# Kernel tuning notes

Hardware: AMD Instinct MI355X
Metric: run time of the kernel (lower is better)

The kernel has to match this reference:

```python
import jax, jax.numpy as jnp
import numpy as np

B, CIN, H, W = 4, 64, 128, 128
COUT, KH, KW = 64, 3, 3
STRIDE, PAD, DIL = 1, 1, 1
GROUPS, DG = 1, 1


def setup_inputs() -> dict:
    key = jax.random.key(0)
    k1, k2, k3, k4 = jax.random.split(key, 4)
    K = KH * KW
    x = jax.random.normal(k1, (B, CIN, H, W), jnp.float32)
    offset = jax.random.normal(k2, (B, 2 * DG * K, H, W), jnp.float32)
    mask = jax.random.uniform(k3, (B, DG * K, H, W), jnp.float32)
    stdv = 1.0 / np.sqrt(CIN * KH * KW)
    weight = jax.random.uniform(k4, (COUT, CIN // GROUPS, KH, KW), jnp.float32, -stdv, stdv)
    bias = jnp.zeros((COUT,), jnp.float32)
    return {"x": x, "offset": offset, "mask": mask, "weight": weight, "bias": bias}


def _deform_conv2d(x, offset, mask, weight, bias):
    Bn, C, Hi, Wi = x.shape
    Co, Cg_in, kh, kw = weight.shape
    K = kh * kw
    Ho = (Hi + 2 * PAD - DIL * (kh - 1) - 1) // STRIDE + 1
    Wo = (Wi + 2 * PAD - DIL * (kw - 1) - 1) // STRIDE + 1
    Cg = C // DG  # channels per deform group

    # offset channel layout: (deform_group, tap, {dy, dx})
    off = offset.reshape(Bn, DG, K, 2, Ho, Wo)
    dy, dx = off[:, :, :, 0], off[:, :, :, 1]          # [B, DG, K, Ho, Wo]
    m = mask.reshape(Bn, DG, K, Ho, Wo)

    ky = (jnp.arange(K) // kw) * DIL                    # tap row offsets
    kx = (jnp.arange(K) % kw) * DIL                     # tap col offsets
    oy = jnp.arange(Ho) * STRIDE - PAD
    ox = jnp.arange(Wo) * STRIDE - PAD
    py = dy + ky[None, None, :, None, None] + oy[None, None, None, :, None]
    px = dx + kx[None, None, :, None, None] + ox[None, None, None, None, :]

    y0f = jnp.floor(py)
    x0f = jnp.floor(px)
    wy = py - y0f
    wx = px - x0f
    y0 = y0f.astype(jnp.int32)
    x0 = x0f.astype(jnp.int32)

    xf = x.reshape(Bn, DG, Cg, Hi * Wi)

    def gather(yi, xi):
        # bilinear corner gather with zero padding outside the image
        valid = ((yi >= 0) & (yi < Hi) & (xi >= 0) & (xi < Wi)).astype(x.dtype)
        idx = jnp.clip(yi, 0, Hi - 1) * Wi + jnp.clip(xi, 0, Wi - 1)
        idx = jnp.broadcast_to(idx.reshape(Bn, DG, 1, -1), (Bn, DG, Cg, K * Ho * Wo))
        g = jnp.take_along_axis(xf, idx, axis=-1)
        return g.reshape(Bn, DG, Cg, K, Ho, Wo) * valid[:, :, None]

    v = (gather(y0, x0) * ((1 - wy) * (1 - wx))[:, :, None]
         + gather(y0, x0 + 1) * ((1 - wy) * wx)[:, :, None]
         + gather(y0 + 1, x0) * (wy * (1 - wx))[:, :, None]
         + gather(y0 + 1, x0 + 1) * (wy * wx)[:, :, None])
    v = v * m[:, :, None]                               # modulation, [B, DG, Cg, K, Ho, Wo]

    v = v.reshape(Bn, GROUPS, C // GROUPS, K, Ho, Wo)
    wflat = weight.reshape(GROUPS, Co // GROUPS, Cg_in, K)
    out = jnp.einsum('bgckhw,gock->bgohw', v, wflat).reshape(Bn, Co, Ho, Wo)
    return out + bias[None, :, None, None]


def reference(x, offset, mask, weight, bias):
    return _deform_conv2d(x, offset, mask, weight, bias)
```

## Files before the change

### kernel.cpp

```cpp
#include <hip/hip_runtime.h>

#define B_    4
#define CIN_  64
#define H_    128
#define W_    128
#define COUT_ 64
#define HW    (H_*W_)
#define KPOS  576

typedef __attribute__((ext_vector_type(8))) short    bf16x8;
typedef __attribute__((ext_vector_type(4))) short    bf16x4;
typedef __attribute__((ext_vector_type(4))) float    f32x4;
typedef __attribute__((ext_vector_type(4))) _Float16 f16x4;
typedef __attribute__((ext_vector_type(8))) _Float16 f16x8;

static __device__ __forceinline__ unsigned short f2bf(float f) {
    union { float f; unsigned u; } a; a.f = f;
    unsigned r = a.u + 0x7fffu + ((a.u >> 16) & 1u);
    return (unsigned short)(r >> 16);
}
static __device__ __forceinline__ float bfl(unsigned u) {
    union { unsigned x; float f; } a; a.x = u << 16; return a.f;
}

#define XT_HALFS   4194304
#define WP_HALFS   36864
#define META_CNT   (B_*9*HW)
#define OFFS_BYTE  ((XT_HALFS + WP_HALFS) * 2)
#define WTS_BYTE   (OFFS_BYTE + META_CNT * 4)
#define WS_NEED3   ((size_t)(WTS_BYTE + META_CNT * 8))

__global__ __launch_bounds__(256)
void prep_all(const float* __restrict__ x,
              const float* __restrict__ offset,
              const float* __restrict__ mask,
              const float* __restrict__ w,
              _Float16* __restrict__ xT,
              _Float16* __restrict__ wt,
              unsigned* __restrict__ mOffs,
              f16x4* __restrict__ mWts)
{
    const int bid = blockIdx.x;
    const int t   = threadIdx.x;

    if (bid < 512) {
        __shared__ _Float16 ld[64 * 132];
        const int b = bid >> 7;
        const int y = bid & 127;
        const float* src = x + (size_t)b * 64 * HW + y * W_;
        #pragma unroll
        for (int i = 0; i < 8; ++i) {
            const int e4 = (t + i * 256) * 4;
            const int c  = e4 >> 7;
            const int x0 = e4 & 127;
            const float4 v = *(const float4*)(src + (size_t)c * HW + x0);
            _Float16* d = &ld[c * 132 + x0];
            d[0] = (_Float16)v.x; d[1] = (_Float16)v.y;
            d[2] = (_Float16)v.z; d[3] = (_Float16)v.w;
        }
        __syncthreads();
        _Float16* dst = xT + ((size_t)b * HW + (size_t)y * W_) * 64;
        #pragma unroll
        for (int i = 0; i < 4; ++i) {
            const int o    = (t + i * 256) * 8;
            const int xcol = o >> 6;
            const int c0   = o & 63;
            union { f16x8 v; _Float16 u[8]; } pk;
            #pragma unroll
            for (int j = 0; j < 8; ++j) pk.u[j] = ld[(c0 + j) * 132 + xcol];
            *(f16x8*)(dst + o) = pk.v;
        }
    } else if (bid < 2816) {
        const int i  = (bid - 512) * 256 + t;
        const int gp = i & (HW - 1);
        const int bk = i >> 14;
        const int b  = bk / 9;
        const int k  = bk - b * 9;
        const int ho = gp >> 7, wo = gp & 127;
        const float dy = offset[(size_t)(b * 18 + 2 * k) * HW + gp];
        const float dx = offset[(size_t)(b * 18 + 2 * k + 1) * HW + gp];
        const float mm = mask[(size_t)bk * HW + gp];
        const float py  = dy + (float)(k / 3) + (float)(ho - 1);
        const float pxx = dx + (float)(k % 3) + (float)(wo - 1);
        const float y0f = floorf(py), x0f = floorf(pxx);
        const float wy = py - y0f, wx = pxx - x0f;
        const int y0 = (int)y0f, x0 = (int)x0f;
        const int y1 = y0 + 1,  x1 = x0 + 1;
        const bool vy0 = (y0 >= 0) & (y0 < H_), vy1 = (y1 >= 0) & (y1 < H_);
        const bool vx0 = (x0 >= 0) & (x0 < W_), vx1 = (x1 >= 0) & (x1 < W_);
        const int cy0 = min(max(y0, 0), H_-1), cy1 = min(max(y1, 0), H_-1);
        const int cx0 = min(max(x0, 0), W_-1), cx1 = min(max(x1, 0), W_-1);
        mOffs[i] = (unsigned)cy0 | ((unsigned)cy1 << 8)
                 | ((unsigned)cx0 << 16) | ((unsigned)cx1 << 24);
        f16x4 wv;
        wv[0] = (_Float16)((vy0 && vx0) ? (1.f - wy) * (1.f - wx) * mm : 0.f);
        wv[1] = (_Float16)((vy0 && vx1) ? (1.f - wy) * wx * mm         : 0.f);
        wv[2] = (_Float16)((vy1 && vx0) ? wy * (1.f - wx) * mm         : 0.f);
        wv[3] = (_Float16)((vy1 && vx1) ? wy * wx * mm                 : 0.f);
        mWts[i] = wv;
    } else {
        const int i = (bid - 2816) * 256 + t;
        if (i < 9 * 64 * 64) {
            const int k  = i >> 12;
            const int r  = i & 4095;
            const int co = r >> 6;
            const int c  = r & 63;
            wt[i] = (_Float16)w[co * KPOS + c * 9 + k];
        }
    }
}

__global__ __launch_bounds__(256, 4)
void dcn_f16(const _Float16* __restrict__ xT,
             const unsigned* __restrict__ mOffs,
             const f16x4* __restrict__ mWts,
             const float* __restrict__ bias,
             const _Float16* __restrict__ wprep,
             float* __restrict__ out)
{
    __shared__ _Float16 vP[2][64][72];
    __shared__ _Float16 Wk[2][64][72];

    const int t   = threadIdx.x;
    const int bid = blockIdx.x;
    const int wk  = ((bid & 7) << 7) | (bid >> 3);
    const int xh  = wk & 1;
    const int ho  = (wk >> 1) & 127;
    const int b   = wk >> 8;
    const int cq  = t >> 6;
    const int lane = t & 63;
    const int pxl  = lane >> 2;
    const int coct = lane & 3;

    f32x4 acc[4];
    #pragma unroll
    for (int i = 0; i < 4; ++i) acc[i] = (f32x4){0.f, 0.f, 0.f, 0.f};

    const _Float16* xTb = xT + (size_t)b * HW * 64;
    const int gp    = ho * W_ + xh * 64 + cq * 16 + pxl;
    const int mbase = (b * 9) << 14;

    unsigned pk9[9]; f16x4 wh9[9];
    #pragma unroll
    for (int k = 0; k < 9; ++k) {
        const int mi = mbase + (k << 14) + gp;
        pk9[k] = mOffs[mi];
        wh9[k] = mWts[mi];
    }

    f16x8 cr[2][4];

    auto ld = [&](int k) {
        const unsigned pk = pk9[k];
        const int y0c = pk & 255,         y1c = (pk >> 8) & 255;
        const int x0c = (pk >> 16) & 255, x1c = (int)(pk >> 24);
        const int cho = coct * 8;
        const int p00 = (((y0c << 7) | x0c) << 6) + cho;
        const int p01 = (((y0c << 7) | x1c) << 6) + cho;
        const int p10 = (((y1c << 7) | x0c) << 6) + cho;
        const int p11 = (((y1c << 7) | x1c) << 6) + cho;
        #pragma unroll
        for (int pass = 0; pass < 2; ++pass) {
            const int o = pass * 32;
            cr[pass][0] = *(const f16x8*)(xTb + p00 + o);
            cr[pass][1] = *(const f16x8*)(xTb + p01 + o);
            cr[pass][2] = *(const f16x8*)(xTb + p10 + o);
            cr[pass][3] = *(const f16x8*)(xTb + p11 + o);
        }
    };

    auto fin = [&](int k) {
        const int s = k & 1;
        {
            const int j  = t * 8;
            *(f16x8*)&Wk[s][j >> 6][j & 63] =
                *(const f16x8*)(wprep + k * 4096 + j);
            const int j2 = 2048 + j;
            *(f16x8*)&Wk[s][j2 >> 6][j2 & 63] =
                *(const f16x8*)(wprep + k * 4096 + j2);
        }
        const _Float16 w0 = wh9[k][0];
        const _Float16 w1 = wh9[k][1];
        const _Float16 w2 = wh9[k][2];
        const _Float16 w3 = wh9[k][3];
        #pragma unroll
        for (int pass = 0; pass < 2; ++pass) {
            f16x8 a = cr[pass][0] * w0 + cr[pass][1] * w1
                    + cr[pass][2] * w2 + cr[pass][3] * w3;
            *(f16x8*)&vP[s][cq * 16 + pxl][pass * 32 + coct * 8] = a;
        }
    };

    auto domfma = [&](int k) {
        const int s  = k & 1;
        const int ra = cq * 16 + (lane & 15);
        const int kc = (lane >> 4) * 8;
        #pragma unroll
        for (int ks = 0; ks < 2; ++ks) {
            const int kcol = ks * 32 + kc;
            const f16x8 a = *(const f16x8*)&vP[s][ra][kcol];
            #pragma unroll
            for (int nt = 0; nt < 4; ++nt) {
                const f16x8 bb = *(const f16x8*)&Wk[s][nt * 16 + (lane & 15)][kcol];
                acc[nt] = __builtin_amdgcn_mfma_f32_16x16x32_f16(a, bb, acc[nt], 0, 0, 0);
            }
        }
    };

    ld(0);
    fin(0);
    __syncthreads();
    #pragma unroll
    for (int k = 0; k < 9; ++k) {
        if (k < 8) ld(k + 1);
        domfma(k);
        if (k < 8) fin(k + 1);
        __syncthreads();
    }

    const int px0 = cq * 16 + (lane >> 4) * 4;
    #pragma unroll
    for (int nt = 0; nt < 4; ++nt) {
        const int co = nt * 16 + (lane & 15);
        const float bb = bias[co];
        float4 r;
        r.x = acc[nt][0] + bb;
        r.y = acc[nt][1] + bb;
        r.z = acc[nt][2] + bb;
        r.w = acc[nt][3] + bb;
        *(float4*)&out[(((size_t)b * COUT_ + co) * H_ + ho) * W_ + xh * 64 + px0] = r;
    }
}

__global__ __launch_bounds__(256)
void xpose_bf16(const float* __restrict__ x, unsigned short* __restrict__ xT)
{
    __shared__ unsigned short ld[64 * 132];
    const int t   = threadIdx.x;
    const int blk = blockIdx.x;
    const int b   = blk >> 7;
    const int y   = blk & 127;
    const float* src = x + (size_t)b * 64 * HW + y * W_;
    #pragma unroll
    for (int i = 0; i < 8; ++i) {
        const int e4 = (t + i * 256) * 4;
        const int c  = e4 >> 7;
        const int x0 = e4 & 127;
        const float4 v = *(const float4*)(src + (size_t)c * HW + x0);
        unsigned short* d = &ld[c * 132 + x0];
        d[0] = f2bf(v.x); d[1] = f2bf(v.y); d[2] = f2bf(v.z); d[3] = f2bf(v.w);
    }
    __syncthreads();
    unsigned short* dst = xT + ((size_t)b * HW + (size_t)y * W_) * 64;
    #pragma unroll
    for (int i = 0; i < 4; ++i) {
        const int o    = (t + i * 256) * 8;
        const int xcol = o >> 6;
        const int c0   = o & 63;
        union { bf16x8 v; unsigned short u[8]; } pk;
        #pragma unroll
        for (int j = 0; j < 8; ++j) pk.u[j] = ld[(c0 + j) * 132 + xcol];
        *(bf16x8*)(dst + o) = pk.v;
    }
}

__global__ void prep_weight_fb(const float* __restrict__ w,
                               unsigned short* __restrict__ wt)
{
    const int i = blockIdx.x * 256 + threadIdx.x;
    if (i >= 9 * 64 * 64) return;
    const int k  = i >> 12;
    const int r  = i & 4095;
    const int co = r >> 6;
    const int c  = r & 63;
    wt[i] = f2bf(w[co * KPOS + c * 9 + k]);
}

__global__ __launch_bounds__(256, 4)
void dcn_mfma_nhwc(const unsigned short* __restrict__ xT,
                   const float* __restrict__ offset,
                   const float* __restrict__ mask,
                   const float* __restrict__ bias,
                   const unsigned short* __restrict__ wprep,
                   float* __restrict__ out)
{
    __shared__ unsigned short vP[2][64][72];
    __shared__ unsigned short Wk[2][64][72];
    const int t   = threadIdx.x;
    const int bid = blockIdx.x;
    const int wk  = ((bid & 7) << 7) | (bid >> 3);
    const int xh  = wk & 1;
    const int ho  = (wk >> 1) & 127;
    const int b   = wk >> 8;
    const int cq  = t >> 6;
    const int lane = t & 63;
    const int px_sub = lane >> 4;
    const int c4     = lane & 15;
    f32x4 acc[4];
    #pragma unroll
    for (int i = 0; i < 4; ++i) acc[i] = (f32x4){0.f, 0.f, 0.f, 0.f};
    const unsigned short* xTb = xT + (size_t)b * HW * 64;

    auto stage = [&](int k, int s) {
        int   idxs[4][4];
        float wts [4][4];
        #pragma unroll
        for (int it = 0; it < 4; ++it) {
            const int pl = (cq << 4) | (it << 2) | px_sub;
            const int wo = xh * 64 + pl;
            const int obase = ((b * 18 + 2 * k) * H_ + ho) * W_ + wo;
            const float dy = offset[obase];
            const float dx = offset[obase + HW];
            const float mm = mask[((b * 9 + k) * H_ + ho) * W_ + wo];
            const float py  = dy + (float)(k / 3) + (float)(ho - 1);
            const float pxx = dx + (float)(k % 3) + (float)(wo - 1);
            const float y0f = floorf(py), x0f = floorf(pxx);
            const float wy = py - y0f, wx = pxx - x0f;
            const int y0 = (int)y0f, x0 = (int)x0f;
            const int y1 = y0 + 1,  x1 = x0 + 1;
            const bool vy0 = (y0 >= 0) & (y0 < H_), vy1 = (y1 >= 0) & (y1 < H_);
            const bool vx0 = (x0 >= 0) & (x0 < W_), vx1 = (x1 >= 0) & (x1 < W_);
            const int cy0 = min(max(y0, 0), H_-1), cy1 = min(max(y1, 0), H_-1);
            const int cx0 = min(max(x0, 0), W_-1), cx1 = min(max(x1, 0), W_-1);
            idxs[it][0] = (cy0 * W_ + cx0) << 6;
            idxs[it][1] = (cy0 * W_ + cx1) << 6;
            idxs[it][2] = (cy1 * W_ + cx0) << 6;
            idxs[it][3] = (cy1 * W_ + cx1) << 6;
            wts[it][0] = (vy0 && vx0) ? (1.f - wy) * (1.f - wx) * mm : 0.f;
            wts[it][1] = (vy0 && vx1) ? (1.f - wy) * wx * mm         : 0.f;
            wts[it][2] = (vy1 && vx0) ? wy * (1.f - wx) * mm         : 0.f;
            wts[it][3] = (vy1 && vx1) ? wy * wx * mm                 : 0.f;
        }
        bf16x4 cr[4][4];
        #pragma unroll
        for (int it = 0; it < 4; ++it)
            #pragma unroll
            for (int cn = 0; cn < 4; ++cn)
                cr[it][cn] = *(const bf16x4*)(xTb + idxs[it][cn] + (c4 << 2));
        #pragma unroll
        for (int q = 0; q < 2; ++q) {
            const int j  = q * 2048 + t * 8;
            *(bf16x8*)&Wk[s][j >> 6][j & 63] = *(const bf16x8*)(wprep + k * 4096 + j);
        }
        #pragma unroll
        for (int it = 0; it < 4; ++it) {
            const int pl = (cq << 4) | (it << 2) | px_sub;
            union { bf16x4 v; unsigned short u[4]; } pk;
            #pragma unroll
            for (int j = 0; j < 4; ++j) {
                union { short s; unsigned short u; } s0{cr[it][0][j]}, s1{cr[it][1][j]},
                                                     s2{cr[it][2][j]}, s3{cr[it][3][j]};
                const float v = wts[it][0] * bfl(s0.u) + wts[it][1] * bfl(s1.u)
                              + wts[it][2] * bfl(s2.u) + wts[it][3] * bfl(s3.u);
                pk.u[j] = f2bf(v);
            }
            *(bf16x4*)&vP[s][pl][c4 << 2] = pk.v;
        }
    };
    auto domfma = [&](int s) {
        const int ra = cq * 16 + (lane & 15);
        const int kc = (lane >> 4) * 8;
        #pragma unroll
        for (int ks = 0; ks < 2; ++ks) {
            const int kcol = ks * 32 + kc;
            const bf16x8 a = *(const bf16x8*)&vP[s][ra][kcol];
            #pragma unroll
            for (int nt = 0; nt < 4; ++nt) {
                const bf16x8 bb = *(const bf16x8*)&Wk[s][nt * 16 + (lane & 15)][kcol];
                acc[nt] = __builtin_amdgcn_mfma_f32_16x16x32_bf16(a, bb, acc[nt], 0, 0, 0);
            }
        }
    };
    stage(0, 0);
    __syncthreads();
    for (int k = 0; k < 9; ++k) {
        const int s = k & 1;
        if (k < 8) stage(k + 1, s ^ 1);
        domfma(s);
        __syncthreads();
    }
    const int px0 = cq * 16 + (lane >> 4) * 4;
    #pragma unroll
    for (int nt = 0; nt < 4; ++nt) {
        const int co = nt * 16 + (lane & 15);
        const float bb = bias[co];
        float4 r;
        r.x = acc[nt][0] + bb;
        r.y = acc[nt][1] + bb;
        r.z = acc[nt][2] + bb;
        r.w = acc[nt][3] + bb;
        *(float4*)&out[(((size_t)b * COUT_ + co) * H_ + ho) * W_ + xh * 64 + px0] = r;
    }
}

extern "C" void kernel_launch(void* const* d_in, const int* in_sizes, int n_in,
                              void* d_out, int out_size, void* d_ws, size_t ws_size,
                              hipStream_t stream)
{
    const float* x      = (const float*)d_in[0];
    const float* offset = (const float*)d_in[1];
    const float* mask   = (const float*)d_in[2];
    const float* weight = (const float*)d_in[3];
    const float* bias   = (const float*)d_in[4];
    float* out = (float*)d_out;

    dim3 block(256);
    dim3 grid(B_ * H_ * 2);

    if (ws_size >= WS_NEED3) {
        _Float16* xT    = (_Float16*)d_ws;
        _Float16* wprep = xT + XT_HALFS;
        unsigned* mOffs = (unsigned*)((char*)d_ws + OFFS_BYTE);
        f16x4*    mWts  = (f16x4*)  ((char*)d_ws + WTS_BYTE);
        prep_all<<<dim3(2960), block, 0, stream>>>(x, offset, mask, weight,
                                                   xT, wprep, mOffs, mWts);
        dcn_f16<<<grid, block, 0, stream>>>(xT, mOffs, mWts, bias, wprep, out);
    } else {
        unsigned short* xTb   = (unsigned short*)d_ws;
        unsigned short* wprep = xTb + XT_HALFS;
        xpose_bf16<<<dim3(B_ * H_), block, 0, stream>>>(x, xTb);
        prep_weight_fb<<<dim3(144), block, 0, stream>>>(weight, wprep);
        dcn_mfma_nhwc<<<grid, block, 0, stream>>>(xTb, offset, mask, bias, wprep, out);
    }
}
```

Before: 37.55 us.

## Deepen gather pipeline to two taps ahead with double-buffered register corners

Restructures the per-tap loop so the offset/mask metadata and bilinear corner gathers are issued two taps ahead, held in double-buffered register sets, instead of preloading all nine metadata entries and gathering one tap ahead. Weight tile global loads are split from their LDS stores so they are also issued a tap early, and the final redundant barrier is removed. The aim is to hide global gather latency behind more MFMA work, at the cost of higher register pressure from doubling the corner buffers, which could lower occupancy.

After: 35.15 us. 1.07x faster.

```diff
diff --git a/kernel.cpp b/kernel.cpp
--- a/kernel.cpp
+++ b/kernel.cpp
@@ -140,18 +140,17 @@
     const int gp    = ho * W_ + xh * 64 + cq * 16 + pxl;
     const int mbase = (b * 9) << 14;
 
-    unsigned pk9[9]; f16x4 wh9[9];
-    #pragma unroll
-    for (int k = 0; k < 9; ++k) {
+    unsigned mO[2]; f16x4 mW[2];
+    f16x8 cr[2][2][4];
+    f16x8 wa0, wa1;
+
+    auto metald = [&](int k, int s) {
         const int mi = mbase + (k << 14) + gp;
-        pk9[k] = mOffs[mi];
-        wh9[k] = mWts[mi];
-    }
-
-    f16x8 cr[2][4];
-
-    auto ld = [&](int k) {
-        const unsigned pk = pk9[k];
+        mO[s] = mOffs[mi];
+        mW[s] = mWts[mi];
+    };
+    auto gather = [&](int k, int s) {
+        const unsigned pk = mO[s];
         const int y0c = pk & 255,         y1c = (pk >> 8) & 255;
         const int x0c = (pk >> 16) & 255, x1c = (int)(pk >> 24);
         const int cho = coct * 8;
@@ -162,35 +161,33 @@
         #pragma unroll
         for (int pass = 0; pass < 2; ++pass) {
             const int o = pass * 32;
-            cr[pass][0] = *(const f16x8*)(xTb + p00 + o);
-            cr[pass][1] = *(const f16x8*)(xTb + p01 + o);
-            cr[pass][2] = *(const f16x8*)(xTb + p10 + o);
-            cr[pass][3] = *(const f16x8*)(xTb + p11 + o);
-        }
-    };
-
-    auto fin = [&](int k) {
-        const int s = k & 1;
-        {
-            const int j  = t * 8;
-            *(f16x8*)&Wk[s][j >> 6][j & 63] =
-                *(const f16x8*)(wprep + k * 4096 + j);
-            const int j2 = 2048 + j;
-            *(f16x8*)&Wk[s][j2 >> 6][j2 & 63] =
-                *(const f16x8*)(wprep + k * 4096 + j2);
-        }
-        const _Float16 w0 = wh9[k][0];
-        const _Float16 w1 = wh9[k][1];
-        const _Float16 w2 = wh9[k][2];
-        const _Float16 w3 = wh9[k][3];
+            cr[s][pass][0] = *(const f16x8*)(xTb + p00 + o);
+            cr[s][pass][1] = *(const f16x8*)(xTb + p01 + o);
+            cr[s][pass][2] = *(const f16x8*)(xTb + p10 + o);
+            cr[s][pass][3] = *(const f16x8*)(xTb + p11 + o);
+        }
+    };
+    auto wkload = [&](int k) {
+        const int j = t * 8;
+        wa0 = *(const f16x8*)(wprep + k * 4096 + j);
+        wa1 = *(const f16x8*)(wprep + k * 4096 + 2048 + j);
+    };
+    auto finish = [&](int k, int s) {
+        const int j  = t * 8;
+        *(f16x8*)&Wk[s][j >> 6][j & 63] = wa0;
+        const int j2 = 2048 + j;
+        *(f16x8*)&Wk[s][j2 >> 6][j2 & 63] = wa1;
+        const _Float16 w0 = mW[s][0];
+        const _Float16 w1 = mW[s][1];
+        const _Float16 w2 = mW[s][2];
+        const _Float16 w3 = mW[s][3];
         #pragma unroll
         for (int pass = 0; pass < 2; ++pass) {
-            f16x8 a = cr[pass][0] * w0 + cr[pass][1] * w1
-                    + cr[pass][2] * w2 + cr[pass][3] * w3;
+            f16x8 a = cr[s][pass][0] * w0 + cr[s][pass][1] * w1
+                    + cr[s][pass][2] * w2 + cr[s][pass][3] * w3;
             *(f16x8*)&vP[s][cq * 16 + pxl][pass * 32 + coct * 8] = a;
         }
     };
-
     auto domfma = [&](int k) {
         const int s  = k & 1;
         const int ra = cq * 16 + (lane & 15);
@@ -207,15 +204,25 @@
         }
     };
 
-    ld(0);
-    fin(0);
+    metald(0, 0);
+    metald(1, 1);
+    gather(0, 0);
+    gather(1, 1);
+    wkload(0);
+    finish(0, 0);
     __syncthreads();
+
     #pragma unroll
     for (int k = 0; k < 9; ++k) {
-        if (k < 8) ld(k + 1);
+        const int s = k & 1;
+        if (k < 8) wkload(k + 1);
+        if (k < 7) metald(k + 2, s);
         domfma(k);
-        if (k < 8) fin(k + 1);
-        __syncthreads();
+        if (k < 7) gather(k + 2, s);
+        if (k < 8) {
+            finish(k + 1, s ^ 1);
+            __syncthreads();
+        }
     }
 
     const int px0 = cq * 16 + (lane >> 4) * 4;
```
